# Kernel tuning notes

Hardware: AMD Instinct MI355X
Metric: run time of the kernel (lower is better)

Reference implementation:

```python
import jax, jax.numpy as jnp
import numpy as np

N = 100000   # nodes per graph
E = 1600000  # edges (avg degree 16)
B = 2        # num_graph (batch)
F_IN = 116   # num_input
EMB = 12     # embedding dim
H = 128      # hidden_size


def setup_inputs() -> dict:
    key = jax.random.key(0)
    ks = jax.random.split(key, 8)
    node = jax.random.normal(ks[0], (B, N, F_IN), dtype=jnp.float32)
    node_type = jax.random.randint(ks[1], (N,), 0, 8, dtype=jnp.int32)
    edge_index = jax.random.randint(ks[2], (2, E), 0, N, dtype=jnp.int32)
    embed = jax.random.normal(ks[3], (8, EMB), dtype=jnp.float32)
    d1 = F_IN + EMB
    W1 = jax.random.normal(ks[4], (d1, H), dtype=jnp.float32) / np.sqrt(d1)
    b1 = jnp.zeros((H,), dtype=jnp.float32)
    W2 = jax.random.normal(ks[5], (H, H), dtype=jnp.float32) / np.sqrt(H)
    b2 = jnp.zeros((H,), dtype=jnp.float32)
    return {"node": node, "node_type": node_type, "edge_index": edge_index,
            "embed": embed, "W1": W1, "b1": b1, "W2": W2, "b2": b2}


def _gcn_conv(x, src, dst, W, b):
    """PyG GCNConv: symmetric norm with self-loops, linear (no lin bias), bias after agg.
    x: [B, N, F]; src/dst: [E] int; W: [F, H]; b: [H]."""
    n = x.shape[1]
    # degree over (A + I), computed on destination nodes
    deg = jnp.zeros((n,), x.dtype).at[dst].add(1.0) + 1.0
    dis = jax.lax.rsqrt(deg)  # deg^{-1/2}
    xw = jnp.einsum('bnf,fh->bnh', x, W)          # [B, N, H]
    norm = dis[src] * dis[dst]                    # [E]
    msgs = xw[:, src, :] * norm[None, :, None]    # [B, E, H]
    agg = jax.vmap(lambda m: jax.ops.segment_sum(m, dst, num_segments=n))(msgs)
    agg = agg + xw * (dis * dis)[None, :, None]   # self-loop contribution
    return agg + b


def reference(node, node_type, edge_index, embed, W1, b1, W2, b2):
    src, dst = edge_index[0], edge_index[1]
    emb = embed[node_type]                                      # [N, EMB]
    b = node.shape[0]
    emb_b = jnp.broadcast_to(emb[None], (b,) + emb.shape)       # repeat over batch
    x = jnp.concatenate([node, emb_b], axis=2)                  # [B, N, F_IN+EMB]
    x = jax.nn.relu(_gcn_conv(x, src, dst, W1, b1))
    # F.dropout in eval mode is identity
    x = _gcn_conv(x, src, dst, W2, b2)
    return jnp.mean(x, axis=1)                                  # [B, H]
```

## Files before the change

### kernel.cpp

```cpp
#include <hip/hip_runtime.h>
#include <stdint.h>

typedef unsigned int uint32;
typedef unsigned short ushort16;
typedef __attribute__((ext_vector_type(8))) short bf16x8;
typedef __attribute__((ext_vector_type(4))) float f32x4;
typedef __attribute__((ext_vector_type(2))) float f32x2;

#define F_IN 116
#define HID  128
#define EMBD 12
#define IDX24 0x00FFFFFFu
#define BCAP 4608
#define PCAP 8448

__device__ __forceinline__ ushort16 f2bf(float f) {
    uint32 x = __float_as_uint(f);
    uint32 r = (x + 0x7fffu + ((x >> 16) & 1u)) >> 16;
    return (ushort16)r;
}

__global__ void k_setup(const float* __restrict__ W1, ushort16* __restrict__ W1s,
                        int* __restrict__ bcurD, int* __restrict__ bcurS,
                        float* __restrict__ partial, uint32* __restrict__ xwzrow,
                        int* __restrict__ csrz, int N, int K) {
    int tid = blockIdx.x * 256 + threadIdx.x;
    if (tid < K) { bcurD[tid] = tid * BCAP; bcurS[tid] = tid * BCAP; }
    if (blockIdx.x == 0) {
        partial[threadIdx.x] = 0.f;
        if (threadIdx.x < 64) xwzrow[threadIdx.x] = 0u;
        if (threadIdx.x < 16) csrz[threadIdx.x] = N;
    }
    if (tid < 2048) {
        int q = tid & 3, n = (tid >> 2) & 15, t = (tid >> 6) & 7, kc = (tid >> 9) & 3;
        int chunk = ((kc * 8 + t) * 64 + n * 4 + q);
#pragma unroll
        for (int j = 0; j < 8; ++j) {
            int k = kc * 32 + q * 8 + j;
            W1s[chunk * 8 + j] = f2bf(W1[k * HID + t * 16 + n]);
        }
    }
}

__global__ __launch_bounds__(256) void k_bin(
    const int* __restrict__ src, const int* __restrict__ dst,
    int* __restrict__ bcurD, int* __restrict__ bcurS,
    uint32* __restrict__ ebufD, uint32* __restrict__ ebufS, int E) {
    __shared__ int lhD[512], lbD[512], lhS[512], lbS[512];
    const int tid = threadIdx.x;
    const int e0 = blockIdx.x * 4096;
    const int eend = min(e0 + 4096, E);
    for (int i = tid; i < 512; i += 256) { lhD[i] = 0; lhS[i] = 0; }
    __syncthreads();
    for (int e = e0 + tid; e < eend; e += 256) {
        atomicAdd(&lhD[dst[e] >> 8], 1);
        atomicAdd(&lhS[src[e] >> 8], 1);
    }
    __syncthreads();
    const int rot = (blockIdx.x * 277) & 511;
#pragma unroll
    for (int i = 0; i < 2; ++i) {
        int k = (rot + tid + i * 256) & 511;
        int c = lhD[k]; lbD[k] = c ? atomicAdd(&bcurD[k], c) : 0; lhD[k] = 0;
        int d = lhS[k]; lbS[k] = d ? atomicAdd(&bcurS[k], d) : 0; lhS[k] = 0;
    }
    __syncthreads();
    for (int e = e0 + tid; e < eend; e += 256) {
        int s = src[e], d = dst[e];
        int bkD = d >> 8;
        int p = lbD[bkD] + atomicAdd(&lhD[bkD], 1);
        if (p < (bkD + 1) * BCAP) ebufD[p] = ((uint32)(d & 255) << 24) | (uint32)s;
        int bkS = s >> 8;
        int p2 = lbS[bkS] + atomicAdd(&lhS[bkS], 1);
        if (p2 < (bkS + 1) * BCAP) ebufS[p2] = ((uint32)(s & 255) << 24) | (uint32)d;
    }
}

__global__ __launch_bounds__(256) void k_csr(
    const uint32* __restrict__ ebufD, const int* __restrict__ bcurD,
    int4* __restrict__ meta, float* __restrict__ dis,
    int* __restrict__ csr, int N, int ZROW) {
    __shared__ int cnt[256];
    __shared__ int cur[256];
    __shared__ int lst[256];
    __shared__ int ps[256];
    const int b = blockIdx.x, tid = threadIdx.x;
    const int r0 = b * BCAP;
    const int r1 = min(bcurD[b], r0 + BCAP);
    cnt[tid] = 0;
    __syncthreads();
    for (int p = r0 + tid; p < r1; p += 256)
        atomicAdd(&cnt[ebufD[p] >> 24], 1);
    __syncthreads();
    const int pl = (cnt[tid] + 15) & ~15;
    ps[tid] = pl;
    __syncthreads();
    for (int off = 1; off < 256; off <<= 1) {
        int t = (tid >= off) ? ps[tid - off] : 0;
        __syncthreads();
        ps[tid] += t;
        __syncthreads();
    }
    const int start = b * PCAP + ps[tid] - pl;
    lst[tid] = start;
    cur[tid] = start;
    const int n = (b << 8) + tid;
    float dl = rsqrtf(1.0f + (float)cnt[tid]);
    if (n < N) {
        dis[n] = dl;
        meta[n] = make_int4(start, pl >> 4, __float_as_int(dl), 0);
    }
    __syncthreads();
    for (int p = r0 + tid; p < r1; p += 256) {
        uint32 v = ebufD[p];
        csr[atomicAdd(&cur[v >> 24], 1)] = (int)(v & IDX24);
    }
    __syncthreads();
    {
        int end = lst[tid] + pl;
        for (int p = cur[tid]; p < end; ++p) csr[p] = ZROW;
    }
}

__global__ __launch_bounds__(256) void k_souts(
    const uint32* __restrict__ ebufS, const int* __restrict__ bcurS,
    const float* __restrict__ dis, int4* __restrict__ meta, int N) {
    __shared__ float lso[256];
    const int b = blockIdx.x, tid = threadIdx.x;
    const int r0 = b * BCAP;
    const int r1 = min(bcurS[b], r0 + BCAP);
    lso[tid] = 0.f;
    __syncthreads();
    for (int p = r0 + tid; p < r1; p += 256) {
        uint32 v = ebufS[p];
        atomicAdd(&lso[v >> 24], dis[v & IDX24]);
    }
    __syncthreads();
    int n = (b << 8) + tid;
    if (n < N) meta[n].w = __float_as_int(lso[tid]);
}

__global__ __launch_bounds__(256, 4) void k_gemm(
    const float* __restrict__ node, const ushort16* __restrict__ W1s,
    const int* __restrict__ ntype, const float* __restrict__ embed,
    const float* __restrict__ dis, uint32* __restrict__ xw8, int N, int M)
{
    __shared__ ushort16 ldsA[4 * 4 * 64 * 8];
    __shared__ float ldis[32];
    const int tid = threadIdx.x;
    const int row0 = blockIdx.x * 64;

    if (tid < 32) {
        int n = (row0 >> 1) + tid;
        ldis[tid] = (n < N) ? dis[n] : 0.f;
    }

    const int g = tid & 31;
    const int kc0 = g >> 3, q0 = (g >> 1) & 3, half = g & 1;
#pragma unroll
    for (int j = 0; j < 8; ++j) {
        int r = (tid >> 5) + j * 8;
        int m = row0 + r;
        int n = m >> 1, b = m & 1;
        float4 v = make_float4(0.f, 0.f, 0.f, 0.f);
        if (n < N) {
            if (g < 29) v = *(const float4*)(node + ((size_t)b * N + n) * F_IN + g * 4);
            else        v = *(const float4*)(embed + ntype[n] * EMBD + (g - 29) * 4);
        }
        uint32 u0 = (uint32)f2bf(v.x) | ((uint32)f2bf(v.y) << 16);
        uint32 u1 = (uint32)f2bf(v.z) | ((uint32)f2bf(v.w) << 16);
        int mt = r >> 4, mloc = r & 15;
        int chunk = (mt * 4 + kc0) * 64 + mloc * 4 + q0;
        *(uint2*)&ldsA[chunk * 8 + half * 4] = make_uint2(u0, u1);
    }
    __syncthreads();

    const int lane = tid & 63;
    const int w = tid >> 6;
    const int fragsel = (lane & 15) * 4 + (lane >> 4);

    f32x4 acc[8];
#pragma unroll
    for (int ct = 0; ct < 8; ++ct) acc[ct] = (f32x4){0.f, 0.f, 0.f, 0.f};

#pragma unroll
    for (int kc = 0; kc < 4; ++kc) {
        bf16x8 bfr = *(const bf16x8*)&ldsA[(((w * 4 + kc) * 64) + fragsel) * 8];
#pragma unroll
        for (int ct = 0; ct < 8; ++ct) {
            bf16x8 afr = *(const bf16x8*)&W1s[(((kc * 8 + ct) * 64) + fragsel) * 8];
            acc[ct] = __builtin_amdgcn_mfma_f32_16x16x32_bf16(afr, bfr, acc[ct], 0, 0, 0);
        }
    }

    const int row = lane & 15, q = lane >> 4;
    int m = row0 + w * 16 + row;
    if (m < M) {
        float dn = ldis[(w * 16 + row) >> 1];
        uint32* rowp = xw8 + (size_t)m * 32;
#pragma unroll
        for (int ct = 0; ct < 8; ++ct) {
            f32x4 a = acc[ct];
            int u = __builtin_amdgcn_cvt_pk_fp8_f32(a[0] * dn, a[1] * dn, 0, false);
            u = __builtin_amdgcn_cvt_pk_fp8_f32(a[2] * dn, a[3] * dn, u, true);
            rowp[ct * 4 + q] = (uint32)u;
        }
    }
}

__global__ __launch_bounds__(256, 4) void k_gather(
    const uint32* __restrict__ xw8, const int* __restrict__ csr,
    const int4* __restrict__ meta, const float* __restrict__ b1,
    float* __restrict__ partial, int n0, int n1, int ZT)
{
    __shared__ float sm[4][256];
    const int tid  = threadIdx.x;
    const int lane = tid & 63;
    const int wid  = tid >> 6;
    const int wv = (blockIdx.x * blockDim.x + tid) >> 6;
    const int nw = (gridDim.x * blockDim.x) >> 6;
    const int c0 = (lane & 31) * 4;
    const int slot = (lane >> 5) * HID + c0;
    const float bb0 = b1[c0], bb1 = b1[c0 + 1], bb2 = b1[c0 + 2], bb3 = b1[c0 + 3];

    float p0 = 0.f, p1 = 0.f, p2 = 0.f, p3 = 0.f;

    for (int n = n0 + wv * 2; n < n1; n += nw * 2) {
        const int ns = __builtin_amdgcn_readfirstlane(n);
        const int has2 = (ns + 1 < n1);
        const int4 m1 = meta[ns];
        const int4 m2 = has2 ? meta[ns + 1] : make_int4(0, 0, 0, 0);
        const int st1 = m1.x, c1 = m1.y;
        const float dn1 = __int_as_float(m1.z), so1 = __int_as_float(m1.w);
        const int st2 = m2.x, c2 = m2.y;
        const float dn2 = __int_as_float(m2.z), so2 = __int_as_float(m2.w);

        uint32 sv1 = xw8[(size_t)ns * 64 + lane];
        uint32 sv2 = has2 ? xw8[((size_t)ns + 1) * 64 + lane] : 0u;
        f32x2 lo1 = __builtin_amdgcn_cvt_pk_f32_fp8(sv1, false);
        f32x2 hi1 = __builtin_amdgcn_cvt_pk_f32_fp8(sv1, true);
        f32x2 lo2 = __builtin_amdgcn_cvt_pk_f32_fp8(sv2, false);
        f32x2 hi2 = __builtin_amdgcn_cvt_pk_f32_fp8(sv2, true);
        float a10 = lo1.x, a11 = lo1.y, a12 = hi1.x, a13 = hi1.y;
        float a20 = lo2.x, a21 = lo2.y, a22 = hi2.x, a23 = hi2.y;

        int o1 = (c1 > 0) ? st1 : ZT;
        int o2 = (c2 > 0) ? st2 : ZT;
        int4 A0 = *(const int4*)&csr[o1];      int4 A1 = *(const int4*)&csr[o1 + 4];
        int4 A2 = *(const int4*)&csr[o1 + 8];  int4 A3 = *(const int4*)&csr[o1 + 12];
        int4 B0 = *(const int4*)&csr[o2];      int4 B1 = *(const int4*)&csr[o2 + 4];
        int4 B2 = *(const int4*)&csr[o2 + 8];  int4 B3 = *(const int4*)&csr[o2 + 12];

        const int jm = max(c1, c2);
        for (int j = 0; j < jm; ++j) {
            uint32 w1[16], w2[16];
            w1[0]  = xw8[(size_t)A0.x * 64 + lane];
            w1[1]  = xw8[(size_t)A0.y * 64 + lane];
            w1[2]  = xw8[(size_t)A0.z * 64 + lane];
            w1[3]  = xw8[(size_t)A0.w * 64 + lane];
            w1[4]  = xw8[(size_t)A1.x * 64 + lane];
            w1[5]  = xw8[(size_t)A1.y * 64 + lane];
            w1[6]  = xw8[(size_t)A1.z * 64 + lane];
            w1[7]  = xw8[(size_t)A1.w * 64 + lane];
            w1[8]  = xw8[(size_t)A2.x * 64 + lane];
            w1[9]  = xw8[(size_t)A2.y * 64 + lane];
            w1[10] = xw8[(size_t)A2.z * 64 + lane];
            w1[11] = xw8[(size_t)A2.w * 64 + lane];
            w1[12] = xw8[(size_t)A3.x * 64 + lane];
            w1[13] = xw8[(size_t)A3.y * 64 + lane];
            w1[14] = xw8[(size_t)A3.z * 64 + lane];
            w1[15] = xw8[(size_t)A3.w * 64 + lane];
            w2[0]  = xw8[(size_t)B0.x * 64 + lane];
            w2[1]  = xw8[(size_t)B0.y * 64 + lane];
            w2[2]  = xw8[(size_t)B0.z * 64 + lane];
            w2[3]  = xw8[(size_t)B0.w * 64 + lane];
            w2[4]  = xw8[(size_t)B1.x * 64 + lane];
            w2[5]  = xw8[(size_t)B1.y * 64 + lane];
            w2[6]  = xw8[(size_t)B1.z * 64 + lane];
            w2[7]  = xw8[(size_t)B1.w * 64 + lane];
            w2[8]  = xw8[(size_t)B2.x * 64 + lane];
            w2[9]  = xw8[(size_t)B2.y * 64 + lane];
            w2[10] = xw8[(size_t)B2.z * 64 + lane];
            w2[11] = xw8[(size_t)B2.w * 64 + lane];
            w2[12] = xw8[(size_t)B3.x * 64 + lane];
            w2[13] = xw8[(size_t)B3.y * 64 + lane];
            w2[14] = xw8[(size_t)B3.z * 64 + lane];
            w2[15] = xw8[(size_t)B3.w * 64 + lane];

            const int j1 = j + 1;
            o1 = (j1 < c1) ? st1 + j1 * 16 : ZT;
            o2 = (j1 < c2) ? st2 + j1 * 16 : ZT;
            A0 = *(const int4*)&csr[o1];      A1 = *(const int4*)&csr[o1 + 4];
            A2 = *(const int4*)&csr[o1 + 8];  A3 = *(const int4*)&csr[o1 + 12];
            B0 = *(const int4*)&csr[o2];      B1 = *(const int4*)&csr[o2 + 4];
            B2 = *(const int4*)&csr[o2 + 8];  B3 = *(const int4*)&csr[o2 + 12];

            asm volatile("" ::: "memory");

#pragma unroll
            for (int k = 0; k < 16; ++k) {
                f32x2 lo = __builtin_amdgcn_cvt_pk_f32_fp8(w1[k], false);
                f32x2 hi = __builtin_amdgcn_cvt_pk_f32_fp8(w1[k], true);
                a10 += lo.x; a11 += lo.y; a12 += hi.x; a13 += hi.y;
            }
#pragma unroll
            for (int k = 0; k < 16; ++k) {
                f32x2 lo = __builtin_amdgcn_cvt_pk_f32_fp8(w2[k], false);
                f32x2 hi = __builtin_amdgcn_cvt_pk_f32_fp8(w2[k], true);
                a20 += lo.x; a21 += lo.y; a22 += hi.x; a23 += hi.y;
            }
        }

        float cf1 = dn1 * (dn1 + so1);
        p0 = fmaf(cf1, fmaxf(fmaf(dn1, a10, bb0), 0.f), p0);
        p1 = fmaf(cf1, fmaxf(fmaf(dn1, a11, bb1), 0.f), p1);
        p2 = fmaf(cf1, fmaxf(fmaf(dn1, a12, bb2), 0.f), p2);
        p3 = fmaf(cf1, fmaxf(fmaf(dn1, a13, bb3), 0.f), p3);
        if (has2) {
            float cf2 = dn2 * (dn2 + so2);
            p0 = fmaf(cf2, fmaxf(fmaf(dn2, a20, bb0), 0.f), p0);
            p1 = fmaf(cf2, fmaxf(fmaf(dn2, a21, bb1), 0.f), p1);
            p2 = fmaf(cf2, fmaxf(fmaf(dn2, a22, bb2), 0.f), p2);
            p3 = fmaf(cf2, fmaxf(fmaf(dn2, a23, bb3), 0.f), p3);
        }
    }

    *(float4*)&sm[wid][slot] = make_float4(p0, p1, p2, p3);
    __syncthreads();
    if (tid < 256) {
        float s = sm[0][tid] + sm[1][tid] + sm[2][tid] + sm[3][tid];
        atomicAdd(&partial[tid], s);
    }
}

__global__ void k_final(const float* __restrict__ partial, const float* __restrict__ W2,
                        const float* __restrict__ b2, float* __restrict__ out, float invN) {
    int tid = threadIdx.x;
    int b = tid >> 7, h = tid & 127;
    float acc = 0.f;
#pragma unroll 8
    for (int k = 0; k < HID; ++k)
        acc += partial[b * HID + k] * W2[k * HID + h];
    out[tid] = acc * invN + b2[h];
}

extern "C" void kernel_launch(void* const* d_in, const int* in_sizes, int n_in,
                              void* d_out, int out_size, void* d_ws, size_t ws_size,
                              hipStream_t stream) {
    const float* node  = (const float*)d_in[0];
    const int*   ntype = (const int*)d_in[1];
    const int*   eidx  = (const int*)d_in[2];
    const float* embed = (const float*)d_in[3];
    const float* W1    = (const float*)d_in[4];
    const float* b1    = (const float*)d_in[5];
    const float* W2    = (const float*)d_in[6];
    const float* b2    = (const float*)d_in[7];
    float* out = (float*)d_out;

    const int N  = in_sizes[1];
    const int E  = in_sizes[2] / 2;
    const int B  = in_sizes[0] / (N * F_IN);
    const int M  = B * N;
    const int K  = (N + 255) >> 8;

    const int* src = eidx;
    const int* dst = eidx + E;

    char* ws = (char*)d_ws;
    size_t off = 0;
    auto alloc = [&](size_t bytes) -> void* {
        void* p = ws + off;
        off += (bytes + 255) & ~(size_t)255;
        return p;
    };
    uint32*   xw8     = (uint32*)alloc((size_t)(M + 2) * 128);
    int*      csr     = (int*)alloc(((size_t)K * PCAP + 16) * sizeof(int));
    uint32*   ebufD   = (uint32*)alloc((size_t)K * BCAP * sizeof(uint32));
    uint32*   ebufS   = (uint32*)alloc((size_t)K * BCAP * sizeof(uint32));
    int4*     meta    = (int4*)alloc((size_t)N * sizeof(int4));
    float*    dis     = (float*)alloc((size_t)N * sizeof(float));
    ushort16* W1s     = (ushort16*)alloc(4 * 8 * 64 * 8 * sizeof(ushort16));
    int*      bcurD   = (int*)alloc((size_t)K * sizeof(int));
    int*      bcurS   = (int*)alloc((size_t)K * sizeof(int));
    float*    partial = (float*)alloc(2 * HID * sizeof(float));

    const int ZT = K * PCAP;
    const int Nh = (N / 2 + 1) & ~1;

    k_setup<<<8, 256, 0, stream>>>(W1, W1s, bcurD, bcurS, partial,
                                   xw8 + (size_t)N * 64, csr + (size_t)ZT, N, K);
    k_bin<<<(E + 4095) / 4096, 256, 0, stream>>>(src, dst, bcurD, bcurS, ebufD, ebufS, E);
    k_csr<<<K, 256, 0, stream>>>(ebufD, bcurD, meta, dis, csr, N, N);
    k_souts<<<K, 256, 0, stream>>>(ebufS, bcurS, dis, meta, N);
    k_gemm<<<(M + 63) / 64, 256, 0, stream>>>(node, W1s, ntype, embed, dis, xw8, N, M);
    k_gather<<<1536, 256, 0, stream>>>(xw8, csr, meta, b1, partial, 0, Nh, ZT);
    k_gather<<<1536, 256, 0, stream>>>(xw8, csr, meta, b1, partial, Nh, N, ZT);
    k_final<<<1, 256, 0, stream>>>(partial, W2, b2, out, 1.0f / (float)N);
}
```

Measured before the change: 404.5 us.

## Make GEMM persistent with LDS-resident W1 and permuted columns for vector stores

The layer-1 GEMM becomes a persistent kernel on a fixed 768-block grid that loops over row tiles. Each block loads the bf16-packed W1 fragments into LDS once, instead of reading them from global memory on every tile. W1's column order is permuted during packing so each lane's eight fp8 output words are contiguous and can be written with two 16-byte stores instead of eight scattered 4-byte stores. The node loads are batched into registers before bf16 conversion, and an asm memory barrier is removed from the gather loop. The cost is 32 KB of extra LDS per block and the loss of the occupancy hint, which may reduce overlap.

```diff
diff --git a/kernel.cpp b/kernel.cpp
--- a/kernel.cpp
+++ b/kernel.cpp
@@ -14,10 +14,9 @@
 #define BCAP 4608
 #define PCAP 8448
 
-__device__ __forceinline__ ushort16 f2bf(float f) {
+__device__ __forceinline__ uint32 f2bf(float f) {
     uint32 x = __float_as_uint(f);
-    uint32 r = (x + 0x7fffu + ((x >> 16) & 1u)) >> 16;
-    return (ushort16)r;
+    return (x + 0x7fffu + ((x >> 16) & 1u)) >> 16;
 }
 
 __global__ void k_setup(const float* __restrict__ W1, ushort16* __restrict__ W1s,
@@ -34,10 +33,11 @@
     if (tid < 2048) {
         int q = tid & 3, n = (tid >> 2) & 15, t = (tid >> 6) & 7, kc = (tid >> 9) & 3;
         int chunk = ((kc * 8 + t) * 64 + n * 4 + q);
+        int h = ((n >> 2) << 5) + t * 4 + (n & 3);
 #pragma unroll
         for (int j = 0; j < 8; ++j) {
             int k = kc * 32 + q * 8 + j;
-            W1s[chunk * 8 + j] = f2bf(W1[k * HID + t * 16 + n]);
+            W1s[chunk * 8 + j] = (ushort16)f2bf(W1[k * HID + h]);
         }
     }
 }
@@ -140,71 +140,94 @@
     if (n < N) meta[n].w = __float_as_int(lso[tid]);
 }
 
-__global__ __launch_bounds__(256, 4) void k_gemm(
+__global__ __launch_bounds__(256) void k_gemm(
     const float* __restrict__ node, const ushort16* __restrict__ W1s,
     const int* __restrict__ ntype, const float* __restrict__ embed,
-    const float* __restrict__ dis, uint32* __restrict__ xw8, int N, int M)
+    const float* __restrict__ dis, uint32* __restrict__ xw8, int N, int M, int T)
 {
     __shared__ ushort16 ldsA[4 * 4 * 64 * 8];
-    __shared__ float ldis[32];
+    __shared__ uint4    ldsW[2048];
+    __shared__ float    ldis[32];
     const int tid = threadIdx.x;
-    const int row0 = blockIdx.x * 64;
-
-    if (tid < 32) {
-        int n = (row0 >> 1) + tid;
-        ldis[tid] = (n < N) ? dis[n] : 0.f;
+
+    {
+        const uint4* Wg = (const uint4*)W1s;
+#pragma unroll
+        for (int i = 0; i < 8; ++i) ldsW[i * 256 + tid] = Wg[i * 256 + tid];
     }
 
     const int g = tid & 31;
     const int kc0 = g >> 3, q0 = (g >> 1) & 3, half = g & 1;
-#pragma unroll
-    for (int j = 0; j < 8; ++j) {
-        int r = (tid >> 5) + j * 8;
-        int m = row0 + r;
-        int n = m >> 1, b = m & 1;
-        float4 v = make_float4(0.f, 0.f, 0.f, 0.f);
-        if (n < N) {
-            if (g < 29) v = *(const float4*)(node + ((size_t)b * N + n) * F_IN + g * 4);
-            else        v = *(const float4*)(embed + ntype[n] * EMBD + (g - 29) * 4);
-        }
-        uint32 u0 = (uint32)f2bf(v.x) | ((uint32)f2bf(v.y) << 16);
-        uint32 u1 = (uint32)f2bf(v.z) | ((uint32)f2bf(v.w) << 16);
-        int mt = r >> 4, mloc = r & 15;
-        int chunk = (mt * 4 + kc0) * 64 + mloc * 4 + q0;
-        *(uint2*)&ldsA[chunk * 8 + half * 4] = make_uint2(u0, u1);
-    }
-    __syncthreads();
-
     const int lane = tid & 63;
     const int w = tid >> 6;
     const int fragsel = (lane & 15) * 4 + (lane >> 4);
-
-    f32x4 acc[8];
-#pragma unroll
-    for (int ct = 0; ct < 8; ++ct) acc[ct] = (f32x4){0.f, 0.f, 0.f, 0.f};
-
-#pragma unroll
-    for (int kc = 0; kc < 4; ++kc) {
-        bf16x8 bfr = *(const bf16x8*)&ldsA[(((w * 4 + kc) * 64) + fragsel) * 8];
-#pragma unroll
-        for (int ct = 0; ct < 8; ++ct) {
-            bf16x8 afr = *(const bf16x8*)&W1s[(((kc * 8 + ct) * 64) + fragsel) * 8];
-            acc[ct] = __builtin_amdgcn_mfma_f32_16x16x32_bf16(afr, bfr, acc[ct], 0, 0, 0);
-        }
-    }
-
     const int row = lane & 15, q = lane >> 4;
-    int m = row0 + w * 16 + row;
-    if (m < M) {
-        float dn = ldis[(w * 16 + row) >> 1];
-        uint32* rowp = xw8 + (size_t)m * 32;
-#pragma unroll
-        for (int ct = 0; ct < 8; ++ct) {
-            f32x4 a = acc[ct];
-            int u = __builtin_amdgcn_cvt_pk_fp8_f32(a[0] * dn, a[1] * dn, 0, false);
-            u = __builtin_amdgcn_cvt_pk_fp8_f32(a[2] * dn, a[3] * dn, u, true);
-            rowp[ct * 4 + q] = (uint32)u;
-        }
+
+    for (int t = blockIdx.x; t < T; t += gridDim.x) {
+        const int row0 = t * 64;
+        if (tid < 32) {
+            int n = (row0 >> 1) + tid;
+            ldis[tid] = (n < N) ? dis[n] : 0.f;
+        }
+
+        float4 v[8];
+#pragma unroll
+        for (int j = 0; j < 8; ++j) {
+            int r = (tid >> 5) + j * 8;
+            int m = row0 + r;
+            int n = m >> 1, b = m & 1;
+            float4 val = make_float4(0.f, 0.f, 0.f, 0.f);
+            if (n < N) {
+                const float* ap = (g < 29)
+                    ? node + ((size_t)b * N + n) * F_IN + g * 4
+                    : embed + ntype[n] * EMBD + (g - 29) * 4;
+                val = *(const float4*)ap;
+            }
+            v[j] = val;
+        }
+        asm volatile("" ::: "memory");
+#pragma unroll
+        for (int j = 0; j < 8; ++j) {
+            int r = (tid >> 5) + j * 8;
+            uint32 u0 = f2bf(v[j].x) | (f2bf(v[j].y) << 16);
+            uint32 u1 = f2bf(v[j].z) | (f2bf(v[j].w) << 16);
+            int mt = r >> 4, mloc = r & 15;
+            int chunk = (mt * 4 + kc0) * 64 + mloc * 4 + q0;
+            *(uint2*)&ldsA[chunk * 8 + half * 4] = make_uint2(u0, u1);
+        }
+        __syncthreads();
+
+        f32x4 acc[8];
+#pragma unroll
+        for (int ct = 0; ct < 8; ++ct) acc[ct] = (f32x4){0.f, 0.f, 0.f, 0.f};
+
+#pragma unroll
+        for (int kc = 0; kc < 4; ++kc) {
+            bf16x8 bfr = *(const bf16x8*)&ldsA[(((w * 4 + kc) * 64) + fragsel) * 8];
+#pragma unroll
+            for (int ct = 0; ct < 8; ++ct) {
+                bf16x8 afr = *(const bf16x8*)((const char*)ldsW +
+                                (((kc * 8 + ct) * 64 + fragsel) << 4));
+                acc[ct] = __builtin_amdgcn_mfma_f32_16x16x32_bf16(afr, bfr, acc[ct], 0, 0, 0);
+            }
+        }
+
+        int m = row0 + w * 16 + row;
+        if (m < M) {
+            float dn = ldis[(w * 16 + row) >> 1];
+            uint32 d[8];
+#pragma unroll
+            for (int ct = 0; ct < 8; ++ct) {
+                f32x4 a = acc[ct];
+                int u = __builtin_amdgcn_cvt_pk_fp8_f32(a[0] * dn, a[1] * dn, 0, false);
+                u = __builtin_amdgcn_cvt_pk_fp8_f32(a[2] * dn, a[3] * dn, u, true);
+                d[ct] = (uint32)u;
+            }
+            uint32* rowp = xw8 + (size_t)m * 32 + q * 8;
+            *(uint4*)rowp       = make_uint4(d[0], d[1], d[2], d[3]);
+            *(uint4*)(rowp + 4) = make_uint4(d[4], d[5], d[6], d[7]);
+        }
+        __syncthreads();
     }
 }
 
@@ -295,8 +318,6 @@
             B0 = *(const int4*)&csr[o2];      B1 = *(const int4*)&csr[o2 + 4];
             B2 = *(const int4*)&csr[o2 + 8];  B3 = *(const int4*)&csr[o2 + 12];
 
-            asm volatile("" ::: "memory");
-
 #pragma unroll
             for (int k = 0; k < 16; ++k) {
                 f32x2 lo = __builtin_amdgcn_cvt_pk_f32_fp8(w1[k], false);
@@ -362,6 +383,7 @@
     const int B  = in_sizes[0] / (N * F_IN);
     const int M  = B * N;
     const int K  = (N + 255) >> 8;
+    const int T  = (M + 63) >> 6;
 
     const int* src = eidx;
     const int* dst = eidx + E;
@@ -392,7 +414,7 @@
     k_bin<<<(E + 4095) / 4096, 256, 0, stream>>>(src, dst, bcurD, bcurS, ebufD, ebufS, E);
     k_csr<<<K, 256, 0, stream>>>(ebufD, bcurD, meta, dis, csr, N, N);
     k_souts<<<K, 256, 0, stream>>>(ebufS, bcurS, dis, meta, N);
-    k_gemm<<<(M + 63) / 64, 256, 0, stream>>>(node, W1s, ntype, embed, dis, xw8, N, M);
+    k_gemm<<<768, 256, 0, stream>>>(node, W1s, ntype, embed, dis, xw8, N, M, T);
     k_gather<<<1536, 256, 0, stream>>>(xw8, csr, meta, b1, partial, 0, Nh, ZT);
     k_gather<<<1536, 256, 0, stream>>>(xw8, csr, meta, b1, partial, Nh, N, ZT);
     k_final<<<1, 256, 0, stream>>>(partial, W2, b2, out, 1.0f / (float)N);
```

After: 385.2 us. -4.8%, faster.
